# Optimization experiments

Hardware: AMD Instinct MI355X
Metric: run time of the kernel (lower is better)

The kernel has to match this reference:

```python
import jax, jax.numpy as jnp
import numpy as np

NUM_HEADS = 32
NUM_KV_HEADS = 8
HEAD_DIM = 128  # hidden_size 4096 / 32 heads
ROPE_BASE = 10000.0


def setup_inputs() -> dict:
    key = jax.random.key(0)
    ks = jax.random.split(key, 5)
    H = NUM_HEADS * HEAD_DIM
    KV = NUM_KV_HEADS * HEAD_DIM
    B, S = 1, 2048
    s = 0.02
    return {
        "hidden_states": jax.random.normal(ks[0], (B, S, H), dtype=jnp.float32),
        "Wq": jax.random.normal(ks[1], (H, H), dtype=jnp.float32) * s,
        "Wk": jax.random.normal(ks[2], (H, KV), dtype=jnp.float32) * s,
        "Wv": jax.random.normal(ks[3], (H, KV), dtype=jnp.float32) * s,
        "Wo": jax.random.normal(ks[4], (H, H), dtype=jnp.float32) * s,
    }


def _rope_tables(seq_len, head_dim, dtype):
    inv_freq = 1.0 / (ROPE_BASE ** (jnp.arange(0, head_dim, 2, dtype=jnp.float32) / head_dim))
    freqs = jnp.arange(seq_len, dtype=jnp.float32)[:, None] * inv_freq[None, :]  # [S, hd/2]
    emb = jnp.concatenate([freqs, freqs], axis=-1)  # [S, hd]
    return emb.astype(dtype)  # angles; cos/sin taken by caller


def _rotate_half(x):
    x1, x2 = jnp.split(x, 2, axis=-1)
    return jnp.concatenate([-x2, x1], axis=-1)


def reference(hidden_states, Wq, Wk, Wv, Wo):
    B, S, H = hidden_states.shape
    hd = HEAD_DIM
    scale = hd ** -0.5

    q = (hidden_states @ Wq).reshape(B, S, NUM_HEADS, hd).transpose(0, 2, 1, 3)      # [B,nh,S,hd]
    k = (hidden_states @ Wk).reshape(B, S, NUM_KV_HEADS, hd).transpose(0, 2, 1, 3)   # [B,nkv,S,hd]
    v = (hidden_states @ Wv).reshape(B, S, NUM_KV_HEADS, hd).transpose(0, 2, 1, 3)

    ang = _rope_tables(S, hd, hidden_states.dtype)          # [S, hd]
    cos = jnp.cos(ang)[None, None]                          # [1,1,S,hd]
    sin = jnp.sin(ang)[None, None]
    q = q * cos + _rotate_half(q) * sin
    k = k * cos + _rotate_half(k) * sin

    rep = NUM_HEADS // NUM_KV_HEADS
    if rep > 1:
        k = jnp.repeat(k, rep, axis=1)  # matches torch repeat_interleave on head dim
        v = jnp.repeat(v, rep, axis=1)

    scores = jnp.einsum("bhqd,bhkd->bhqk", q, k) * scale    # [B,nh,S,S]
    causal = jnp.triu(jnp.ones((S, S), dtype=bool), k=1)
    scores = jnp.where(causal[None, None], jnp.float32(-jnp.inf).astype(scores.dtype), scores)
    weights = jax.nn.softmax(scores, axis=-1)
    attn = jnp.einsum("bhqk,bhkd->bhqd", weights, v)        # [B,nh,S,hd]
    out = attn.transpose(0, 2, 1, 3).reshape(B, S, H) @ Wo  # [B,S,H]
    return (out, k, v)
```

## Files before the change

### kernel.cpp

```cpp
#include <hip/hip_runtime.h>
#include <hip/hip_bf16.h>
#include <math.h>

typedef __bf16 bf16_t;
typedef bf16_t bf16x8 __attribute__((ext_vector_type(8)));
typedef bf16_t bf16x4 __attribute__((ext_vector_type(4)));
typedef float  f32x4  __attribute__((ext_vector_type(4)));

#define AS1(p) ((__attribute__((address_space(1))) void*)(p))
#define AS3(p) ((__attribute__((address_space(3))) void*)(p))

__global__ void convert_f32_bf16(const float* __restrict__ in, bf16_t* __restrict__ out)
{
    int i = blockIdx.x * 256 + threadIdx.x;
    float4 v = ((const float4*)in)[i];
    bf16x4 o;
    o[0] = (bf16_t)v.x; o[1] = (bf16_t)v.y; o[2] = (bf16_t)v.z; o[3] = (bf16_t)v.w;
    ((bf16x4*)out)[i] = o;
}

__global__ void transpose_convert(const float* __restrict__ W, bf16_t* __restrict__ Wt,
                                  int K, int N)
{
    __shared__ float tile[32][33];
    const int n0 = blockIdx.x * 32;
    const int k0 = blockIdx.y * 32;
    const int r = threadIdx.x >> 5;
    const int c = threadIdx.x & 31;
    #pragma unroll
    for (int i = 0; i < 32; i += 8)
        tile[r + i][c] = W[(size_t)(k0 + r + i) * N + n0 + c];
    __syncthreads();
    #pragma unroll
    for (int i = 0; i < 32; i += 8)
        Wt[(size_t)(n0 + r + i) * K + k0 + c] = (bf16_t)tile[c][r + i];
}

template <typename OutT>
__global__ __launch_bounds__(256)
void gemm_bt_128(const bf16_t* __restrict__ A, const bf16_t* __restrict__ Bt,
                 OutT* __restrict__ C, int M, int N, int K)
{
    __shared__ bf16_t As[128 * 64];
    __shared__ bf16_t Bs[128 * 64];
    const int t    = threadIdx.x;
    const int lane = t & 63;
    const int wave = t >> 6;

    const int nwg   = gridDim.x * gridDim.y;
    int bid = blockIdx.x + blockIdx.y * gridDim.x;
    const int chunk = nwg >> 3;
    bid = (bid & 7) * chunk + (bid >> 3);
    const int m0 = (bid % gridDim.x) * 128;
    const int n0 = (bid / gridDim.x) * 128;

    const int wm = (wave & 1) * 64;
    const int wn = (wave >> 1) * 64;
    const int lm = lane & 15;
    const int lq = lane >> 4;

    f32x4 acc[4][4] = {};

    const int sr = t >> 3;
    const int sg = ((t & 7) ^ (sr & 7)) * 8;
    const bf16_t* Ag = A  + (size_t)(m0 + sr) * K + sg;
    const bf16_t* Bg = Bt + (size_t)(n0 + sr) * K + sg;
    bf16_t* AsW = As + wave * 512;
    bf16_t* BsW = Bs + wave * 512;

    for (int k0 = 0; k0 < K; k0 += 64) {
        __syncthreads();
        #pragma unroll
        for (int i = 0; i < 4; ++i) {
            __builtin_amdgcn_global_load_lds(AS1(Ag + (size_t)(i * 32) * K + k0),
                                             AS3(AsW + i * 2048), 16, 0, 0);
            __builtin_amdgcn_global_load_lds(AS1(Bg + (size_t)(i * 32) * K + k0),
                                             AS3(BsW + i * 2048), 16, 0, 0);
        }
        __syncthreads();

        #pragma unroll
        for (int kk = 0; kk < 2; ++kk) {
            bf16x8 af[4], bb[4];
            #pragma unroll
            for (int mt = 0; mt < 4; ++mt)
                af[mt] = *(const bf16x8*)(As + (wm + mt * 16 + lm) * 64
                                          + (((kk * 4 + lq) ^ (lm & 7)) * 8));
            #pragma unroll
            for (int nt = 0; nt < 4; ++nt)
                bb[nt] = *(const bf16x8*)(Bs + (wn + nt * 16 + lm) * 64
                                          + (((kk * 4 + lq) ^ (lm & 7)) * 8));
            #pragma unroll
            for (int mt = 0; mt < 4; ++mt)
                #pragma unroll
                for (int nt = 0; nt < 4; ++nt)
                    acc[mt][nt] = __builtin_amdgcn_mfma_f32_16x16x32_bf16(
                        af[mt], bb[nt], acc[mt][nt], 0, 0, 0);
        }
    }

    #pragma unroll
    for (int mt = 0; mt < 4; ++mt) {
        #pragma unroll
        for (int nt = 0; nt < 4; ++nt) {
            const int row = m0 + wm + mt * 16 + lq * 4;
            const int col = n0 + wn + nt * 16 + lm;
            #pragma unroll
            for (int r = 0; r < 4; ++r) {
                float v = acc[mt][nt][r];
                if constexpr (sizeof(OutT) == 2)
                    C[(size_t)(row + r) * N + col] = (OutT)(bf16_t)v;
                else
                    C[(size_t)(row + r) * N + col] = v;
            }
        }
    }
}

__global__ void rope_qk(bf16_t* __restrict__ QKV, float* __restrict__ k_out, int S)
{
    int idx  = blockIdx.x * 256 + threadIdx.x;
    int d    = idx & 63;
    int s    = idx >> 6;
    int head = blockIdx.y;
    float ang = (float)s * exp2f((float)d * -0.20762050593f);
    float sn, cs;
    sincosf(ang, &sn, &cs);
    int col = head < 32 ? head * 128 : 4096 + (head - 32) * 128;
    bf16_t* p = QKV + (size_t)s * 6144 + col;
    float x1 = (float)p[d], x2 = (float)p[d + 64];
    float y1 = x1 * cs - x2 * sn;
    float y2 = x2 * cs + x1 * sn;
    p[d]      = (bf16_t)y1;
    p[d + 64] = (bf16_t)y2;
    if (head >= 32) {
        int g = head - 32;
        #pragma unroll
        for (int j = 0; j < 4; ++j) {
            float* kb = k_out + ((size_t)(g * 4 + j) * S + s) * 128;
            kb[d]      = y1;
            kb[d + 64] = y2;
        }
    }
}

__global__ void v_finish(const bf16_t* __restrict__ QKV, float* __restrict__ v_out,
                         bf16_t* __restrict__ Vt, int S)
{
    __shared__ bf16_t tl[32][33];
    const int s0  = blockIdx.x * 32;
    const int gd0 = blockIdx.y * 32;
    const int r = threadIdx.x >> 5;
    const int c = threadIdx.x & 31;
    #pragma unroll
    for (int i = 0; i < 32; i += 8) {
        int s = s0 + r + i;
        bf16_t v = QKV[(size_t)s * 6144 + 5120 + gd0 + c];
        tl[r + i][c] = v;
        int gd = gd0 + c;
        int g = gd >> 7, d = gd & 127;
        float vf = (float)v;
        #pragma unroll
        for (int j = 0; j < 4; ++j)
            v_out[((size_t)(g * 4 + j) * S + s) * 128 + d] = vf;
    }
    __syncthreads();
    #pragma unroll
    for (int i = 0; i < 32; i += 8)
        Vt[(size_t)(gd0 + r + i) * S + s0 + c] = tl[c][r + i];
}

__global__ void pack_frags(const bf16_t* __restrict__ QKV, const bf16_t* __restrict__ Vt,
                           bf16_t* __restrict__ Kfrag, bf16_t* __restrict__ Vfrag, int S)
{
    const int b  = blockIdx.x;
    const int g  = b >> 5, kt = b & 31;
    const int t  = threadIdx.x;
    bf16x8* Kf = (bf16x8*)Kfrag + (size_t)b * 1024;
    bf16x8* Vf = (bf16x8*)Vfrag + (size_t)b * 1024;
    #pragma unroll
    for (int i = 0; i < 4; ++i) {
        int slot = i * 256 + t;
        int f = slot >> 6, l = slot & 63;
        int kk = f >> 2, nt = f & 3, lm = l & 15, lq = l >> 4;
        Kf[slot] = *(const bf16x8*)(QKV + (size_t)(kt * 64 + nt * 16 + lm) * 6144
                                    + 4096 + g * 128 + kk * 32 + lq * 8);
    }
    #pragma unroll
    for (int i = 0; i < 4; ++i) {
        int slot = i * 256 + t;
        int f = slot >> 6, l = slot & 63;
        int kk = f >> 3, nt = f & 7, lm = l & 15, lq = l >> 4;
        Vf[slot] = *(const bf16x8*)(Vt + (size_t)(g * 128 + nt * 16 + lm) * S
                                    + kt * 64 + kk * 32 + lq * 8);
    }
}

__global__ __launch_bounds__(256, 2)
void attn_fwd(const bf16_t* __restrict__ QKV,
              const bf16_t* __restrict__ Kfrag, const bf16_t* __restrict__ Vfrag,
              bf16_t* __restrict__ O, int S)
{
    const int b    = blockIdx.x;
    const int g    = b & 7;
    const int idx  = b >> 3;
    const int h    = g * 4 + (idx & 3);
    const int c    = 63 - (idx >> 2);
    const int wave = threadIdx.x >> 6;
    const int lane = threadIdx.x & 63;
    const int lm   = lane & 15;
    const int lq   = lane >> 4;
    const int q0   = c * 32;

    __shared__ __align__(16) char smem[19456];
    bf16_t* P  = (bf16_t*)smem + wave * (32 * 72);
    float*  Cb = (float*)smem;
    float*  ml = (float*)(smem + 18432);

    bf16x8 aq[2][4];
    #pragma unroll
    for (int mi = 0; mi < 2; ++mi) {
        const bf16_t* qrow = QKV + (size_t)(q0 + mi * 16 + lm) * 6144 + h * 128;
        #pragma unroll
        for (int kk = 0; kk < 4; ++kk)
            aq[mi][kk] = *(const bf16x8*)(qrow + kk * 32 + lq * 8);
    }

    f32x4 acc[2][8] = {};
    float mrow[2][4], lrow[2][4];
    #pragma unroll
    for (int mi = 0; mi < 2; ++mi)
        #pragma unroll
        for (int r = 0; r < 4; ++r) { mrow[mi][r] = -3.0e38f; lrow[mi][r] = 0.f; }
    const float scale = 0.08838834764831845f;

    const int nkt = (q0 >> 6) + 1;

    for (int kt = wave; kt < nkt; kt += 4) {
        const int k0 = kt * 64;
        const bf16x8* Kf = (const bf16x8*)Kfrag + ((size_t)(g * 32 + kt) << 10);
        const bf16x8* Vf = (const bf16x8*)Vfrag + ((size_t)(g * 32 + kt) << 10);

        bf16x8 bk[4][4];
        #pragma unroll
        for (int kk = 0; kk < 4; ++kk)
            #pragma unroll
            for (int nt = 0; nt < 4; ++nt)
                bk[kk][nt] = Kf[(kk * 4 + nt) * 64 + lane];

        f32x4 sc[2][4] = {};
        #pragma unroll
        for (int kk = 0; kk < 4; ++kk)
            #pragma unroll
            for (int nt = 0; nt < 4; ++nt)
                #pragma unroll
                for (int mi = 0; mi < 2; ++mi)
                    sc[mi][nt] = __builtin_amdgcn_mfma_f32_16x16x32_bf16(
                        aq[mi][kk], bk[kk][nt], sc[mi][nt], 0, 0, 0);

        bf16x8 bv[2][8];
        #pragma unroll
        for (int kk = 0; kk < 2; ++kk)
            #pragma unroll
            for (int nt = 0; nt < 8; ++nt)
                bv[kk][nt] = Vf[(kk * 8 + nt) * 64 + lane];

        #pragma unroll
        for (int mi = 0; mi < 2; ++mi)
            #pragma unroll
            for (int nt = 0; nt < 4; ++nt)
                #pragma unroll
                for (int r = 0; r < 4; ++r)
                    sc[mi][nt][r] *= scale;

        if (kt == nkt - 1) {
            #pragma unroll
            for (int mi = 0; mi < 2; ++mi)
                #pragma unroll
                for (int nt = 0; nt < 4; ++nt) {
                    int col = k0 + nt * 16 + lm;
                    #pragma unroll
                    for (int r = 0; r < 4; ++r) {
                        int row = q0 + mi * 16 + lq * 4 + r;
                        if (col > row) sc[mi][nt][r] = -3.0e38f;
                    }
                }
        }

        #pragma unroll
        for (int mi = 0; mi < 2; ++mi) {
            float tmax[4];
            #pragma unroll
            for (int r = 0; r < 4; ++r)
                tmax[r] = fmaxf(fmaxf(sc[mi][0][r], sc[mi][1][r]),
                                fmaxf(sc[mi][2][r], sc[mi][3][r]));
            #pragma unroll
            for (int off = 1; off < 16; off <<= 1)
                #pragma unroll
                for (int r = 0; r < 4; ++r)
                    tmax[r] = fmaxf(tmax[r], __shfl_xor(tmax[r], off));

            float alpha[4];
            #pragma unroll
            for (int r = 0; r < 4; ++r) {
                float mn = fmaxf(mrow[mi][r], tmax[r]);
                alpha[r] = __expf(mrow[mi][r] - mn);
                mrow[mi][r] = mn;
            }
            float rsum[4] = {0.f, 0.f, 0.f, 0.f};
            #pragma unroll
            for (int nt = 0; nt < 4; ++nt)
                #pragma unroll
                for (int r = 0; r < 4; ++r) {
                    float p = __expf(sc[mi][nt][r] - mrow[mi][r]);
                    sc[mi][nt][r] = p;
                    rsum[r] += p;
                }
            #pragma unroll
            for (int off = 1; off < 16; off <<= 1)
                #pragma unroll
                for (int r = 0; r < 4; ++r)
                    rsum[r] += __shfl_xor(rsum[r], off);
            #pragma unroll
            for (int r = 0; r < 4; ++r)
                lrow[mi][r] = lrow[mi][r] * alpha[r] + rsum[r];
            #pragma unroll
            for (int nt = 0; nt < 8; ++nt)
                #pragma unroll
                for (int r = 0; r < 4; ++r)
                    acc[mi][nt][r] *= alpha[r];

            #pragma unroll
            for (int nt = 0; nt < 4; ++nt)
                #pragma unroll
                for (int r = 0; r < 4; ++r)
                    P[(mi * 16 + lq * 4 + r) * 72 + nt * 16 + lm] = (bf16_t)sc[mi][nt][r];
        }

        bf16x8 ap[2][2];
        #pragma unroll
        for (int mi = 0; mi < 2; ++mi)
            #pragma unroll
            for (int kk = 0; kk < 2; ++kk)
                ap[mi][kk] = *(const bf16x8*)(P + (mi * 16 + lm) * 72 + kk * 32 + lq * 8);

        #pragma unroll
        for (int kk = 0; kk < 2; ++kk)
            #pragma unroll
            for (int nt = 0; nt < 8; ++nt)
                #pragma unroll
                for (int mi = 0; mi < 2; ++mi)
                    acc[mi][nt] = __builtin_amdgcn_mfma_f32_16x16x32_bf16(
                        ap[mi][kk], bv[kk][nt], acc[mi][nt], 0, 0, 0);
    }

    if (lm == 0) {
        #pragma unroll
        for (int mi = 0; mi < 2; ++mi)
            #pragma unroll
            for (int r = 0; r < 4; ++r) {
                int lr = mi * 16 + lq * 4 + r;
                ml[(wave * 2 + 0) * 32 + lr] = mrow[mi][r];
                ml[(wave * 2 + 1) * 32 + lr] = lrow[mi][r];
            }
    }
    __syncthreads();

    float fac[2][4], linv[2][4];
    #pragma unroll
    for (int mi = 0; mi < 2; ++mi)
        #pragma unroll
        for (int r = 0; r < 4; ++r) {
            int lr = mi * 16 + lq * 4 + r;
            float m0 = ml[0 * 32 + lr], m1 = ml[2 * 32 + lr];
            float m2 = ml[4 * 32 + lr], m3 = ml[6 * 32 + lr];
            float mg = fmaxf(fmaxf(m0, m1), fmaxf(m2, m3));
            float ls = ml[1 * 32 + lr] * __expf(m0 - mg)
                     + ml[3 * 32 + lr] * __expf(m1 - mg)
                     + ml[5 * 32 + lr] * __expf(m2 - mg)
                     + ml[7 * 32 + lr] * __expf(m3 - mg);
            fac[mi][r]  = __expf(mrow[mi][r] - mg);
            linv[mi][r] = 1.0f / ls;
        }

    for (int w = 0; w < 3; ++w) {
        if (wave == w) {
            #pragma unroll
            for (int mi = 0; mi < 2; ++mi)
                #pragma unroll
                for (int nt = 0; nt < 8; ++nt)
                    #pragma unroll
                    for (int r = 0; r < 4; ++r) {
                        int lr = mi * 16 + lq * 4 + r;
                        int col = nt * 16 + lm;
                        float v = acc[mi][nt][r] * fac[mi][r];
                        if (w == 0) Cb[lr * 132 + col] = v;
                        else        Cb[lr * 132 + col] += v;
                    }
        }
        __syncthreads();
    }
    if (wave == 3) {
        #pragma unroll
        for (int mi = 0; mi < 2; ++mi)
            #pragma unroll
            for (int nt = 0; nt < 8; ++nt)
                #pragma unroll
                for (int r = 0; r < 4; ++r) {
                    int lr = mi * 16 + lq * 4 + r;
                    int col = nt * 16 + lm;
                    float v = Cb[lr * 132 + col] + acc[mi][nt][r] * fac[mi][r];
                    O[(size_t)(q0 + lr) * 4096 + h * 128 + col] =
                        (bf16_t)(v * linv[mi][r]);
                }
    }
}

extern "C" void kernel_launch(void* const* d_in, const int* in_sizes, int n_in,
                              void* d_out, int out_size, void* d_ws, size_t ws_size,
                              hipStream_t stream)
{
    const float* hidden = (const float*)d_in[0];
    const float* Wq = (const float*)d_in[1];
    const float* Wk = (const float*)d_in[2];
    const float* Wv = (const float*)d_in[3];
    const float* Wo = (const float*)d_in[4];

    const int S = 2048, H = 4096, KV = 1024, NQKV = 6144;

    char* ws = (char*)d_ws;
    bf16_t* hid_b  = (bf16_t*)(ws);
    bf16_t* Wqkv_t = (bf16_t*)(ws + (size_t)(16u  << 20));
    bf16_t* Wo_t   = (bf16_t*)(ws + (size_t)(64u  << 20));
    bf16_t* QKV    = (bf16_t*)(ws + (size_t)(96u  << 20));
    bf16_t* Vt     = (bf16_t*)(ws + (size_t)(120u << 20));
    bf16_t* attn   = (bf16_t*)(ws + (size_t)(124u << 20));
    bf16_t* Kfrag  = (bf16_t*)(ws);
    bf16_t* Vfrag  = (bf16_t*)(ws + (size_t)(4u << 20));

    float* out_o = (float*)d_out;
    float* out_k = out_o + (size_t)S * H;
    float* out_v = out_k + (size_t)32 * S * 128;

    convert_f32_bf16<<<S * H / 4 / 256, 256, 0, stream>>>(hidden, hid_b);
    transpose_convert<<<dim3(H / 32, H / 32), 256, 0, stream>>>(Wq, Wqkv_t, H, H);
    transpose_convert<<<dim3(KV / 32, H / 32), 256, 0, stream>>>(Wk, Wqkv_t + (size_t)4096 * H, H, KV);
    transpose_convert<<<dim3(KV / 32, H / 32), 256, 0, stream>>>(Wv, Wqkv_t + (size_t)5120 * H, H, KV);
    transpose_convert<<<dim3(H / 32, H / 32), 256, 0, stream>>>(Wo, Wo_t, H, H);

    gemm_bt_128<bf16_t><<<dim3(S / 128, NQKV / 128), 256, 0, stream>>>(hid_b, Wqkv_t, QKV, S, NQKV, H);

    rope_qk<<<dim3(S * 64 / 256, 40), 256, 0, stream>>>(QKV, out_k, S);
    v_finish<<<dim3(S / 32, KV / 32), 256, 0, stream>>>(QKV, out_v, Vt, S);
    pack_frags<<<256, 256, 0, stream>>>(QKV, Vt, Kfrag, Vfrag, S);

    attn_fwd<<<2048, 256, 0, stream>>>(QKV, Kfrag, Vfrag, attn, S);

    gemm_bt_128<float><<<dim3(S / 128, H / 128), 256, 0, stream>>>(attn, Wo_t, out_o, S, H, H);
}
```

Baseline: 562.5 us.

## Fuse input prep kernels and merge V transpose into fragment packing

Merges the hidden-state conversion and the four weight transpose-convert launches into one prep_inputs kernel with a block-index dispatch. Also folds v_finish into pack_frags: V is staged through an LDS tile, written out as float4 expanded v_out, and repacked into MFMA fragments, so the intermediate Vt buffer and its global round trip go away. This removes kernel launch overhead and one extra global pass over V. In exchange, pack_kv now writes v_out from only 256 blocks, which may cut parallelism for those stores, and its column-strided LDS reads may cause bank conflicts.

```diff
diff --git a/kernel.cpp b/kernel.cpp
--- a/kernel.cpp
+++ b/kernel.cpp
@@ -10,30 +10,41 @@
 #define AS1(p) ((__attribute__((address_space(1))) void*)(p))
 #define AS3(p) ((__attribute__((address_space(3))) void*)(p))
 
-__global__ void convert_f32_bf16(const float* __restrict__ in, bf16_t* __restrict__ out)
-{
-    int i = blockIdx.x * 256 + threadIdx.x;
-    float4 v = ((const float4*)in)[i];
-    bf16x4 o;
-    o[0] = (bf16_t)v.x; o[1] = (bf16_t)v.y; o[2] = (bf16_t)v.z; o[3] = (bf16_t)v.w;
-    ((bf16x4*)out)[i] = o;
-}
-
-__global__ void transpose_convert(const float* __restrict__ W, bf16_t* __restrict__ Wt,
-                                  int K, int N)
+__global__ void prep_inputs(const float* __restrict__ hidden,
+                            const float* __restrict__ Wq, const float* __restrict__ Wk,
+                            const float* __restrict__ Wv, const float* __restrict__ Wo,
+                            bf16_t* __restrict__ hid_b, bf16_t* __restrict__ Wqkv_t,
+                            bf16_t* __restrict__ Wo_t)
 {
     __shared__ float tile[32][33];
-    const int n0 = blockIdx.x * 32;
+    const int t = threadIdx.x;
+
+    if (blockIdx.x < 64) {
+        int cb = blockIdx.y * 64 + blockIdx.x;
+        int i  = cb * 256 + t;
+        float4 v = ((const float4*)hidden)[i];
+        bf16x4 o;
+        o[0] = (bf16_t)v.x; o[1] = (bf16_t)v.y; o[2] = (bf16_t)v.z; o[3] = (bf16_t)v.w;
+        ((bf16x4*)hid_b)[i] = o;
+        return;
+    }
+
+    const int nxi = blockIdx.x - 64;
+    const float* W; bf16_t* Wt; int N; int n0;
+    if (nxi < 128)      { W = Wq; Wt = Wqkv_t;                             N = 4096; n0 = nxi * 32; }
+    else if (nxi < 160) { W = Wk; Wt = Wqkv_t + (size_t)4096 * 4096;       N = 1024; n0 = (nxi - 128) * 32; }
+    else if (nxi < 192) { W = Wv; Wt = Wqkv_t + (size_t)5120 * 4096;       N = 1024; n0 = (nxi - 160) * 32; }
+    else                { W = Wo; Wt = Wo_t;                               N = 4096; n0 = (nxi - 192) * 32; }
     const int k0 = blockIdx.y * 32;
-    const int r = threadIdx.x >> 5;
-    const int c = threadIdx.x & 31;
+    const int r = t >> 5;
+    const int c = t & 31;
     #pragma unroll
     for (int i = 0; i < 32; i += 8)
         tile[r + i][c] = W[(size_t)(k0 + r + i) * N + n0 + c];
     __syncthreads();
     #pragma unroll
     for (int i = 0; i < 32; i += 8)
-        Wt[(size_t)(n0 + r + i) * K + k0 + c] = (bf16_t)tile[c][r + i];
+        Wt[(size_t)(n0 + r + i) * 4096 + k0 + c] = (bf16_t)tile[c][r + i];
 }
 
 template <typename OutT>
@@ -144,40 +155,16 @@
     }
 }
 
-__global__ void v_finish(const bf16_t* __restrict__ QKV, float* __restrict__ v_out,
-                         bf16_t* __restrict__ Vt, int S)
-{
-    __shared__ bf16_t tl[32][33];
-    const int s0  = blockIdx.x * 32;
-    const int gd0 = blockIdx.y * 32;
-    const int r = threadIdx.x >> 5;
-    const int c = threadIdx.x & 31;
-    #pragma unroll
-    for (int i = 0; i < 32; i += 8) {
-        int s = s0 + r + i;
-        bf16_t v = QKV[(size_t)s * 6144 + 5120 + gd0 + c];
-        tl[r + i][c] = v;
-        int gd = gd0 + c;
-        int g = gd >> 7, d = gd & 127;
-        float vf = (float)v;
-        #pragma unroll
-        for (int j = 0; j < 4; ++j)
-            v_out[((size_t)(g * 4 + j) * S + s) * 128 + d] = vf;
-    }
-    __syncthreads();
-    #pragma unroll
-    for (int i = 0; i < 32; i += 8)
-        Vt[(size_t)(gd0 + r + i) * S + s0 + c] = tl[c][r + i];
-}
-
-__global__ void pack_frags(const bf16_t* __restrict__ QKV, const bf16_t* __restrict__ Vt,
-                           bf16_t* __restrict__ Kfrag, bf16_t* __restrict__ Vfrag, int S)
-{
+__global__ void pack_kv(const bf16_t* __restrict__ QKV, float* __restrict__ v_out,
+                        bf16_t* __restrict__ Kfrag, bf16_t* __restrict__ Vfrag, int S)
+{
+    __shared__ bf16_t Vtile[64][136];
     const int b  = blockIdx.x;
     const int g  = b >> 5, kt = b & 31;
     const int t  = threadIdx.x;
     bf16x8* Kf = (bf16x8*)Kfrag + (size_t)b * 1024;
     bf16x8* Vf = (bf16x8*)Vfrag + (size_t)b * 1024;
+
     #pragma unroll
     for (int i = 0; i < 4; ++i) {
         int slot = i * 256 + t;
@@ -186,13 +173,37 @@
         Kf[slot] = *(const bf16x8*)(QKV + (size_t)(kt * 64 + nt * 16 + lm) * 6144
                                     + 4096 + g * 128 + kk * 32 + lq * 8);
     }
+
+    #pragma unroll
+    for (int i = 0; i < 4; ++i) {
+        int gi = i * 256 + t;
+        int r  = gi >> 4;
+        int cg = gi & 15;
+        bf16x8 q8 = *(const bf16x8*)(QKV + (size_t)(kt * 64 + r) * 6144
+                                     + 5120 + g * 128 + cg * 8);
+        *(bf16x8*)(&Vtile[r][cg * 8]) = q8;
+        float4 lo, hi;
+        lo.x = (float)q8[0]; lo.y = (float)q8[1]; lo.z = (float)q8[2]; lo.w = (float)q8[3];
+        hi.x = (float)q8[4]; hi.y = (float)q8[5]; hi.z = (float)q8[6]; hi.w = (float)q8[7];
+        #pragma unroll
+        for (int jr = 0; jr < 4; ++jr) {
+            float* dst = v_out + ((size_t)(g * 4 + jr) * S + kt * 64 + r) * 128 + cg * 8;
+            ((float4*)dst)[0] = lo;
+            ((float4*)dst)[1] = hi;
+        }
+    }
+    __syncthreads();
+
     #pragma unroll
     for (int i = 0; i < 4; ++i) {
         int slot = i * 256 + t;
         int f = slot >> 6, l = slot & 63;
         int kk = f >> 3, nt = f & 7, lm = l & 15, lq = l >> 4;
-        Vf[slot] = *(const bf16x8*)(Vt + (size_t)(g * 128 + nt * 16 + lm) * S
-                                    + kt * 64 + kk * 32 + lq * 8);
+        bf16x8 o;
+        #pragma unroll
+        for (int j = 0; j < 8; ++j)
+            o[j] = Vtile[kk * 32 + lq * 8 + j][nt * 16 + lm];
+        Vf[slot] = o;
     }
 }
 
@@ -426,14 +437,13 @@
     const float* Wv = (const float*)d_in[3];
     const float* Wo = (const float*)d_in[4];
 
-    const int S = 2048, H = 4096, KV = 1024, NQKV = 6144;
+    const int S = 2048, H = 4096, NQKV = 6144;
 
     char* ws = (char*)d_ws;
     bf16_t* hid_b  = (bf16_t*)(ws);
     bf16_t* Wqkv_t = (bf16_t*)(ws + (size_t)(16u  << 20));
     bf16_t* Wo_t   = (bf16_t*)(ws + (size_t)(64u  << 20));
     bf16_t* QKV    = (bf16_t*)(ws + (size_t)(96u  << 20));
-    bf16_t* Vt     = (bf16_t*)(ws + (size_t)(120u << 20));
     bf16_t* attn   = (bf16_t*)(ws + (size_t)(124u << 20));
     bf16_t* Kfrag  = (bf16_t*)(ws);
     bf16_t* Vfrag  = (bf16_t*)(ws + (size_t)(4u << 20));
@@ -442,17 +452,13 @@
     float* out_k = out_o + (size_t)S * H;
     float* out_v = out_k + (size_t)32 * S * 128;
 
-    convert_f32_bf16<<<S * H / 4 / 256, 256, 0, stream>>>(hidden, hid_b);
-    transpose_convert<<<dim3(H / 32, H / 32), 256, 0, stream>>>(Wq, Wqkv_t, H, H);
-    transpose_convert<<<dim3(KV / 32, H / 32), 256, 0, stream>>>(Wk, Wqkv_t + (size_t)4096 * H, H, KV);
-    transpose_convert<<<dim3(KV / 32, H / 32), 256, 0, stream>>>(Wv, Wqkv_t + (size_t)5120 * H, H, KV);
-    transpose_convert<<<dim3(H / 32, H / 32), 256, 0, stream>>>(Wo, Wo_t, H, H);
+    prep_inputs<<<dim3(384, 128), 256, 0, stream>>>(hidden, Wq, Wk, Wv, Wo,
+                                                    hid_b, Wqkv_t, Wo_t);
 
     gemm_bt_128<bf16_t><<<dim3(S / 128, NQKV / 128), 256, 0, stream>>>(hid_b, Wqkv_t, QKV, S, NQKV, H);
 
     rope_qk<<<dim3(S * 64 / 256, 40), 256, 0, stream>>>(QKV, out_k, S);
-    v_finish<<<dim3(S / 32, KV / 32), 256, 0, stream>>>(QKV, out_v, Vt, S);
-    pack_frags<<<256, 256, 0, stream>>>(QKV, Vt, Kfrag, Vfrag, S);
+    pack_kv<<<256, 256, 0, stream>>>(QKV, out_v, Kfrag, Vfrag, S);
 
     attn_fwd<<<2048, 256, 0, stream>>>(QKV, Kfrag, Vfrag, attn, S);
 
```

New measurement: 577.2 us. +2.6%, slower.
